# Kernel tuning notes

Measured on AMD Instinct MI355X. Metric: run time of the kernel, lower is better.

The kernel has to match this reference:

```python
import jax, jax.numpy as jnp
import numpy as np

N_NODES = 50000
N_EDGES = 1600000
F = 64
EPS = 1e-05


def setup_inputs() -> dict:
    key = jax.random.key(0)
    k1, k2 = jax.random.split(key)
    e = jax.random.normal(k1, (N_EDGES, F), dtype=jnp.float32)
    dst = jax.random.randint(k2, (N_EDGES,), 0, N_NODES, dtype=jnp.int32)
    gamma = jnp.ones((F,), dtype=jnp.float32)
    beta = jnp.zeros((F,), dtype=jnp.float32)
    return {"e": e, "gamma": gamma, "beta": beta, "dst": dst}


def reference(e, gamma, beta, dst):
    # Per-destination-node statistics over the mailbox [deg, F]:
    #   mean over all deg*F elements; std is torch.std -> unbiased (n-1).
    f = e.shape[1]
    ones = jnp.ones((e.shape[0],), dtype=e.dtype)
    deg = jax.ops.segment_sum(ones, dst, num_segments=N_NODES)          # [N]
    cnt = deg * f                                                        # elements per node
    s = jax.ops.segment_sum(e.sum(axis=-1), dst, num_segments=N_NODES)  # [N]
    ss = jax.ops.segment_sum((e * e).sum(axis=-1), dst, num_segments=N_NODES)
    safe_cnt = jnp.maximum(cnt, 1.0)
    mean = s / safe_cnt
    var = (ss - cnt * mean * mean) / jnp.maximum(cnt - 1.0, 1.0)  # unbiased
    std = jnp.sqrt(jnp.maximum(var, 0.0))
    # Broadcast dst stats back per edge and normalize: (e - mean) / (std + eps)
    norm_e = (e - mean[dst][:, None]) / (std[dst][:, None] + EPS)
    return gamma * norm_e + beta
```

## Files before the change

kernel.cpp:

```cpp
#include <hip/hip_runtime.h>

#define N_NODES_C 50000
#define FDIM 64
#define EPS_C 1e-5f

#define PARTS 10
#define NPP 5000
#define SLICE (3 * NPP)
#define BPERP 48
#define SCAT_BLK 512

__global__ void __launch_bounds__(256)
partial_kernel(const float4* __restrict__ e4, float2* __restrict__ partials,
               int nEdges) {
    const int total = nEdges * 16;
    const int stride = gridDim.x * blockDim.x;
    for (int idx = blockIdx.x * blockDim.x + threadIdx.x; idx < total; idx += stride) {
        float4 v = e4[idx];
        float sum = (v.x + v.y) + (v.z + v.w);
        float sq  = (v.x * v.x + v.y * v.y) + (v.z * v.z + v.w * v.w);
#pragma unroll
        for (int m = 1; m < 16; m <<= 1) {
            sum += __shfl_xor(sum, m);
            sq  += __shfl_xor(sq,  m);
        }
        if ((idx & 15) == 0) partials[idx >> 4] = make_float2(sum, sq);
    }
}

__global__ void __launch_bounds__(SCAT_BLK)
scatter_kernel(const int* __restrict__ dst, const float2* __restrict__ partials,
               float* __restrict__ acc, int nEdges) {
    __shared__ float sm[SLICE];
    const int tid = threadIdx.x;
    for (int i = tid; i < SLICE; i += SCAT_BLK) sm[i] = 0.0f;
    __syncthreads();

    const int p  = blockIdx.x / BPERP;
    const int b  = blockIdx.x % BPERP;
    const int lo = p * NPP;

    const int step = BPERP * SCAT_BLK * 4;
    for (int i0 = (b * SCAT_BLK + tid) * 4; i0 < nEdges; i0 += step) {
        if (i0 + 3 < nEdges) {
            int4   d4  = *(const int4*)(dst + i0);
            float4 p01 = *(const float4*)(partials + i0);
            float4 p23 = *(const float4*)(partials + i0 + 2);
            unsigned l0 = (unsigned)(d4.x - lo), l1 = (unsigned)(d4.y - lo);
            unsigned l2 = (unsigned)(d4.z - lo), l3 = (unsigned)(d4.w - lo);
            if (l0 < NPP) { atomicAdd(&sm[l0], p01.x); atomicAdd(&sm[NPP + l0], p01.y); atomicAdd(&sm[2 * NPP + l0], 1.f); }
            if (l1 < NPP) { atomicAdd(&sm[l1], p01.z); atomicAdd(&sm[NPP + l1], p01.w); atomicAdd(&sm[2 * NPP + l1], 1.f); }
            if (l2 < NPP) { atomicAdd(&sm[l2], p23.x); atomicAdd(&sm[NPP + l2], p23.y); atomicAdd(&sm[2 * NPP + l2], 1.f); }
            if (l3 < NPP) { atomicAdd(&sm[l3], p23.z); atomicAdd(&sm[NPP + l3], p23.w); atomicAdd(&sm[2 * NPP + l3], 1.f); }
        } else {
            for (int i = i0; i < nEdges; ++i) {
                unsigned l = (unsigned)(dst[i] - lo);
                if (l < NPP) {
                    float2 pq = partials[i];
                    atomicAdd(&sm[l], pq.x);
                    atomicAdd(&sm[NPP + l], pq.y);
                    atomicAdd(&sm[2 * NPP + l], 1.f);
                }
            }
        }
    }
    __syncthreads();
    float* __restrict__ out = acc + (size_t)blockIdx.x * SLICE;
    for (int i = tid; i < SLICE; i += SCAT_BLK) out[i] = sm[i];
}

__global__ void __launch_bounds__(256)
reduce_finalize_kernel(const float* __restrict__ acc, float2* __restrict__ stats,
                       int nNodes) {
    int n = blockIdx.x * blockDim.x + threadIdx.x;
    if (n >= nNodes) return;
    int p = n / NPP, local = n - p * NPP;
    const float* base = acc + (size_t)(p * BPERP) * SLICE + local;
    float s = 0.f, q = 0.f, dg = 0.f;
#pragma unroll 8
    for (int bb = 0; bb < BPERP; ++bb) {
        const float* a = base + (size_t)bb * SLICE;
        s  += a[0];
        q  += a[NPP];
        dg += a[2 * NPP];
    }
    float cnt  = dg * (float)FDIM;
    float safe = fmaxf(cnt, 1.0f);
    float mean = s / safe;
    float var  = (q - cnt * mean * mean) / fmaxf(cnt - 1.0f, 1.0f);
    float stdv = sqrtf(fmaxf(var, 0.0f));
    stats[n] = make_float2(mean, 1.0f / (stdv + EPS_C));
}

__global__ void __launch_bounds__(256)
norm_kernel(const float4* __restrict__ e4, const int* __restrict__ dst,
            const float2* __restrict__ stats,
            const float4* __restrict__ gamma4, const float4* __restrict__ beta4,
            float4* __restrict__ out4, int nEdges) {
    const int total = nEdges * 16;
    const int stride = gridDim.x * blockDim.x;
    const int sub = (blockIdx.x * blockDim.x + threadIdx.x) & 15;
    const float4 g = gamma4[sub];
    const float4 b = beta4[sub];
    for (int idx = blockIdx.x * blockDim.x + threadIdx.x; idx < total; idx += stride) {
        float2 mi = stats[dst[idx >> 4]];
        float4 v  = e4[idx];
        float4 o;
        o.x = g.x * (v.x - mi.x) * mi.y + b.x;
        o.y = g.y * (v.y - mi.x) * mi.y + b.y;
        o.z = g.z * (v.z - mi.x) * mi.y + b.z;
        o.w = g.w * (v.w - mi.x) * mi.y + b.w;
        out4[idx] = o;
    }
}

extern "C" void kernel_launch(void* const* d_in, const int* in_sizes, int n_in,
                              void* d_out, int out_size, void* d_ws, size_t ws_size,
                              hipStream_t stream) {
    const float* e     = (const float*)d_in[0];
    const float* gamma = (const float*)d_in[1];
    const float* beta  = (const float*)d_in[2];
    const int*   dst   = (const int*)d_in[3];
    const int nEdges = in_sizes[3];
    const int nNodes = N_NODES_C;

    float2* partials = (float2*)d_out;
    float*  acc      = (float*)d_ws;
    float2* stats    = (float2*)(acc + (size_t)PARTS * BPERP * SLICE);

    partial_kernel<<<2048, 256, 0, stream>>>((const float4*)e, partials, nEdges);

    scatter_kernel<<<PARTS * BPERP, SCAT_BLK, 0, stream>>>(dst, partials, acc, nEdges);

    reduce_finalize_kernel<<<(nNodes + 255) / 256, 256, 0, stream>>>(acc, stats, nNodes);

    norm_kernel<<<2048, 256, 0, stream>>>(
        (const float4*)e, dst, stats,
        (const float4*)gamma, (const float4*)beta,
        (float4*)d_out, nEdges);
}
```

Before: 277.1 us.

## Retune scatter partitioning, widen per-thread batch, reverse norm loop order, move partials

Changes the scatter kernel to 16 node partitions of 3125 nodes with 64 blocks each, processes 8 edges per thread per iteration, and adds an occupancy hint to launch bounds. The norm kernel now walks its grid-stride loop in reverse, so it first touches the tail of e, which was read most recently by the partial kernel and may still be in cache. Partials move from the output buffer into workspace. Together these aim to reduce shared-atomic contention per block, raise memory-level parallelism, and improve cache reuse between kernels, at the cost of more workspace traffic in the reduce step (64 slices per node instead of 48).

After: 270.8 us. 1.02x faster.

```diff
diff --git a/kernel.cpp b/kernel.cpp
--- a/kernel.cpp
+++ b/kernel.cpp
@@ -4,11 +4,18 @@
 #define FDIM 64
 #define EPS_C 1e-5f
 
-#define PARTS 10
-#define NPP 5000
+#define PARTS 16
+#define NPP 3125
 #define SLICE (3 * NPP)
-#define BPERP 48
+#define BPERP 64
 #define SCAT_BLK 512
+#define SCAT_GRID (PARTS * BPERP)
+
+#define EDGE_ACC(D, SV, QV)                                            \
+    { unsigned l_ = (unsigned)((D) - lo);                              \
+      if (l_ < NPP) { atomicAdd(&sm[l_], (SV));                        \
+                      atomicAdd(&sm[NPP + l_], (QV));                  \
+                      atomicAdd(&sm[2 * NPP + l_], 1.0f); } }
 
 __global__ void __launch_bounds__(256)
 partial_kernel(const float4* __restrict__ e4, float2* __restrict__ partials,
@@ -28,7 +35,7 @@
     }
 }
 
-__global__ void __launch_bounds__(SCAT_BLK)
+__global__ void __launch_bounds__(SCAT_BLK, 8)
 scatter_kernel(const int* __restrict__ dst, const float2* __restrict__ partials,
                float* __restrict__ acc, int nEdges) {
     __shared__ float sm[SLICE];
@@ -40,33 +47,29 @@
     const int b  = blockIdx.x % BPERP;
     const int lo = p * NPP;
 
-    const int step = BPERP * SCAT_BLK * 4;
-    for (int i0 = (b * SCAT_BLK + tid) * 4; i0 < nEdges; i0 += step) {
-        if (i0 + 3 < nEdges) {
-            int4   d4  = *(const int4*)(dst + i0);
-            float4 p01 = *(const float4*)(partials + i0);
-            float4 p23 = *(const float4*)(partials + i0 + 2);
-            unsigned l0 = (unsigned)(d4.x - lo), l1 = (unsigned)(d4.y - lo);
-            unsigned l2 = (unsigned)(d4.z - lo), l3 = (unsigned)(d4.w - lo);
-            if (l0 < NPP) { atomicAdd(&sm[l0], p01.x); atomicAdd(&sm[NPP + l0], p01.y); atomicAdd(&sm[2 * NPP + l0], 1.f); }
-            if (l1 < NPP) { atomicAdd(&sm[l1], p01.z); atomicAdd(&sm[NPP + l1], p01.w); atomicAdd(&sm[2 * NPP + l1], 1.f); }
-            if (l2 < NPP) { atomicAdd(&sm[l2], p23.x); atomicAdd(&sm[NPP + l2], p23.y); atomicAdd(&sm[2 * NPP + l2], 1.f); }
-            if (l3 < NPP) { atomicAdd(&sm[l3], p23.z); atomicAdd(&sm[NPP + l3], p23.w); atomicAdd(&sm[2 * NPP + l3], 1.f); }
+    const int step = BPERP * SCAT_BLK * 8;
+    for (int i0 = (b * SCAT_BLK + tid) * 8; i0 < nEdges; i0 += step) {
+        if (i0 + 7 < nEdges) {
+            int4   da = *(const int4*)(dst + i0);
+            int4   db = *(const int4*)(dst + i0 + 4);
+            float4 p0 = *(const float4*)(partials + i0);
+            float4 p1 = *(const float4*)(partials + i0 + 2);
+            float4 p2 = *(const float4*)(partials + i0 + 4);
+            float4 p3 = *(const float4*)(partials + i0 + 6);
+            EDGE_ACC(da.x, p0.x, p0.y); EDGE_ACC(da.y, p0.z, p0.w);
+            EDGE_ACC(da.z, p1.x, p1.y); EDGE_ACC(da.w, p1.z, p1.w);
+            EDGE_ACC(db.x, p2.x, p2.y); EDGE_ACC(db.y, p2.z, p2.w);
+            EDGE_ACC(db.z, p3.x, p3.y); EDGE_ACC(db.w, p3.z, p3.w);
         } else {
             for (int i = i0; i < nEdges; ++i) {
-                unsigned l = (unsigned)(dst[i] - lo);
-                if (l < NPP) {
-                    float2 pq = partials[i];
-                    atomicAdd(&sm[l], pq.x);
-                    atomicAdd(&sm[NPP + l], pq.y);
-                    atomicAdd(&sm[2 * NPP + l], 1.f);
-                }
+                float2 pq = partials[i];
+                EDGE_ACC(dst[i], pq.x, pq.y);
             }
         }
     }
     __syncthreads();
-    float* __restrict__ out = acc + (size_t)blockIdx.x * SLICE;
-    for (int i = tid; i < SLICE; i += SCAT_BLK) out[i] = sm[i];
+    float* __restrict__ outp = acc + (size_t)blockIdx.x * SLICE;
+    for (int i = tid; i < SLICE; i += SCAT_BLK) outp[i] = sm[i];
 }
 
 __global__ void __launch_bounds__(256)
@@ -75,14 +78,13 @@
     int n = blockIdx.x * blockDim.x + threadIdx.x;
     if (n >= nNodes) return;
     int p = n / NPP, local = n - p * NPP;
-    const float* base = acc + (size_t)(p * BPERP) * SLICE + local;
+    const float* bptr = acc + (size_t)(p * BPERP) * SLICE + local;
     float s = 0.f, q = 0.f, dg = 0.f;
 #pragma unroll 8
-    for (int bb = 0; bb < BPERP; ++bb) {
-        const float* a = base + (size_t)bb * SLICE;
-        s  += a[0];
-        q  += a[NPP];
-        dg += a[2 * NPP];
+    for (int bb = 0; bb < BPERP; ++bb, bptr += SLICE) {
+        s  += bptr[0];
+        q  += bptr[NPP];
+        dg += bptr[2 * NPP];
     }
     float cnt  = dg * (float)FDIM;
     float safe = fmaxf(cnt, 1.0f);
@@ -97,12 +99,16 @@
             const float2* __restrict__ stats,
             const float4* __restrict__ gamma4, const float4* __restrict__ beta4,
             float4* __restrict__ out4, int nEdges) {
-    const int total = nEdges * 16;
+    const int total  = nEdges * 16;
     const int stride = gridDim.x * blockDim.x;
-    const int sub = (blockIdx.x * blockDim.x + threadIdx.x) & 15;
+    const int gtid   = blockIdx.x * blockDim.x + threadIdx.x;
+    const int sub    = gtid & 15;
     const float4 g = gamma4[sub];
     const float4 b = beta4[sub];
-    for (int idx = blockIdx.x * blockDim.x + threadIdx.x; idx < total; idx += stride) {
+    const int nIter = (total + stride - 1) / stride;
+    for (int it = nIter - 1; it >= 0; --it) {
+        int idx = it * stride + gtid;
+        if (idx >= total) continue;
         float2 mi = stats[dst[idx >> 4]];
         float4 v  = e4[idx];
         float4 o;
@@ -124,16 +130,13 @@
     const int nEdges = in_sizes[3];
     const int nNodes = N_NODES_C;
 
-    float2* partials = (float2*)d_out;
     float*  acc      = (float*)d_ws;
-    float2* stats    = (float2*)(acc + (size_t)PARTS * BPERP * SLICE);
+    float2* stats    = (float2*)(acc + (size_t)SCAT_GRID * SLICE);
+    float2* partials = stats + nNodes;
 
     partial_kernel<<<2048, 256, 0, stream>>>((const float4*)e, partials, nEdges);
-
-    scatter_kernel<<<PARTS * BPERP, SCAT_BLK, 0, stream>>>(dst, partials, acc, nEdges);
-
+    scatter_kernel<<<SCAT_GRID, SCAT_BLK, 0, stream>>>(dst, partials, acc, nEdges);
     reduce_finalize_kernel<<<(nNodes + 255) / 256, 256, 0, stream>>>(acc, stats, nNodes);
-
     norm_kernel<<<2048, 256, 0, stream>>>(
         (const float4*)e, dst, stats,
         (const float4*)gamma, (const float4*)beta,
```
